# Kernel tuning notes

Measured on AMD Instinct MI355X. Metric: run time of the kernel, lower is better.

## Reference

```python
import jax, jax.numpy as jnp
import numpy as np
import math

NB = 4           # num_bands
EPS = 1e-5       # LayerNorm eps


def _dwconv(x, w):
    # depthwise Conv1d, padding=1, kernel=3. x: [b, t, c], w: [c, 1, k]
    c = x.shape[-1]
    y = jax.lax.conv_general_dilated(
        x.transpose(0, 2, 1), w, window_strides=(1,), padding=[(1, 1)],
        dimension_numbers=('NCH', 'OIH', 'NCH'), feature_group_count=c)
    return y.transpose(0, 2, 1)


def _ln(x, g, b):
    m = jnp.mean(x, axis=-1, keepdims=True)
    v = jnp.mean(jnp.square(x - m), axis=-1, keepdims=True)
    return (x - m) * jax.lax.rsqrt(v + EPS) * g + b


def _attn(x, mem, qw, qc, kw, kc, vw, vc, ow, pw, prev_qk):
    # x, mem: [b, w, c]
    b, w, c = x.shape
    d = c // NB
    q = _dwconv(x @ qw.T, qc).reshape(b, w, NB, d).transpose(0, 2, 1, 3)      # [b,nb,w,d]
    k = _dwconv(mem @ kw.T, kc).reshape(b, w, NB, d).transpose(0, 2, 3, 1)    # [b,nb,d,w]
    v = _dwconv(mem @ vw.T, vc).reshape(b, w, NB, d).transpose(0, 2, 1, 3)    # [b,nb,w,d]
    # skewed relative-position bias: matmul + pad + transpose + slice
    p = jnp.einsum('bnwd,dt->bnwt', q, pw[:, :w])                              # [b,nb,w,w]
    p = jnp.pad(p, ((0, 0), (0, 0), (0, 0), (1, 0)))                           # pad last dim left
    p = p.transpose(0, 1, 3, 2)[:, :, 1:, :]                                   # skew
    qk = (jnp.einsum('bnwd,bndt->bnwt', q, k) + p) / math.sqrt(c)
    if prev_qk is not None:
        qk = qk + prev_qk
    a = jnp.einsum('bnwt,bntd->bnwd', jax.nn.softmax(qk, axis=-1), v)
    a = a.transpose(0, 2, 1, 3).reshape(b, w, c)
    return a @ ow.T, qk


def setup_inputs() -> dict:
    key = jax.random.key(0)
    ks = jax.random.split(key, 32)
    B, CH, BINS, W, FF = 4, 8, 1024, 1024, 2048
    s = 0.02
    inp = {
        'x': jax.random.normal(ks[0], (B, CH, BINS, W), jnp.float32),
        'mem': jax.random.normal(ks[1], (B, CH, BINS, W), jnp.float32),
        'prev_qk1': jax.random.normal(ks[2], (B, NB, W, W), jnp.float32),
        'prev_qk2': jax.random.normal(ks[3], (B, NB, W, W), jnp.float32),
        'ip_w': jax.random.normal(ks[4], (CH,), jnp.float32) * s,
        'ip_b': jnp.zeros((1,), jnp.float32),
        'mp_w': jax.random.normal(ks[5], (CH,), jnp.float32) * s,
        'mp_b': jnp.zeros((1,), jnp.float32),
        'ln1_g': jnp.ones((BINS,), jnp.float32), 'ln1_b': jnp.zeros((BINS,), jnp.float32),
        'ln2_g': jnp.ones((BINS,), jnp.float32), 'ln2_b': jnp.zeros((BINS,), jnp.float32),
        'ln3_g': jnp.ones((BINS,), jnp.float32), 'ln3_b': jnp.zeros((BINS,), jnp.float32),
        'a1_qw': jax.random.normal(ks[6], (BINS, BINS), jnp.float32) * s,
        'a1_qc': jax.random.normal(ks[7], (BINS, 1, 3), jnp.float32) * 0.3,
        'a1_kw': jax.random.normal(ks[8], (BINS, BINS), jnp.float32) * s,
        'a1_kc': jax.random.normal(ks[9], (BINS, 1, 3), jnp.float32) * 0.3,
        'a1_vw': jax.random.normal(ks[10], (BINS, BINS), jnp.float32) * s,
        'a1_vc': jax.random.normal(ks[11], (BINS, 1, 3), jnp.float32) * 0.3,
        'a1_ow': jax.random.normal(ks[12], (BINS, BINS), jnp.float32) * s,
        'a1_pw': jax.random.normal(ks[13], (BINS // NB, W), jnp.float32),
        'a2_qw': jax.random.normal(ks[14], (BINS, BINS), jnp.float32) * s,
        'a2_qc': jax.random.normal(ks[15], (BINS, 1, 3), jnp.float32) * 0.3,
        'a2_kw': jax.random.normal(ks[16], (BINS, BINS), jnp.float32) * s,
        'a2_kc': jax.random.normal(ks[17], (BINS, 1, 3), jnp.float32) * 0.3,
        'a2_vw': jax.random.normal(ks[18], (BINS, BINS), jnp.float32) * s,
        'a2_vc': jax.random.normal(ks[19], (BINS, 1, 3), jnp.float32) * 0.3,
        'a2_ow': jax.random.normal(ks[20], (BINS, BINS), jnp.float32) * s,
        'a2_pw': jax.random.normal(ks[21], (BINS // NB, W), jnp.float32),
        'l1_w': jax.random.normal(ks[22], (FF, BINS), jnp.float32) * s,
        'l2_w': jax.random.normal(ks[23], (BINS, FF), jnp.float32) * s,
    }
    return inp


def reference(x, mem, prev_qk1, prev_qk2, ip_w, ip_b, mp_w, mp_b,
              ln1_g, ln1_b, ln2_g, ln2_b, ln3_g, ln3_b,
              a1_qw, a1_qc, a1_kw, a1_kc, a1_vw, a1_vc, a1_ow, a1_pw,
              a2_qw, a2_qc, a2_kw, a2_kc, a2_vw, a2_vc, a2_ow, a2_pw,
              l1_w, l2_w):
    # 1x1 Conv2d to 1 channel then [b, w, bins] layout
    xs = jnp.einsum('bchw,c->bwh', x, ip_w) + ip_b    # [b, w, bins]
    ms = jnp.einsum('bchw,c->bwh', mem, mp_w) + mp_b
    # self-attention with prev_qk residual
    h, qk1 = _attn(_ln(xs, ln1_g, ln1_b), _ln(xs, ln1_g, ln1_b),
                   a1_qw, a1_qc, a1_kw, a1_kc, a1_vw, a1_vc, a1_ow, a1_pw, prev_qk1)
    xs = xs + h
    # cross-attention against mem
    h, qk2 = _attn(_ln(xs, ln2_g, ln2_b), ms,
                   a2_qw, a2_qc, a2_kw, a2_kc, a2_vw, a2_vc, a2_ow, a2_pw, prev_qk2)
    xs = xs + h
    # squared-ReLU FFN
    h = _ln(xs, ln3_g, ln3_b)
    h = jnp.square(jax.nn.relu(h @ l1_w.T)) @ l2_w.T
    xs = xs + h
    out = xs.transpose(0, 2, 1)[:, None]              # [b, 1, bins, w]
    return (out, qk1, qk2)
```

## Files before the change

kernel.cpp:

```cpp
#include <hip/hip_runtime.h>
#include <stdint.h>

typedef unsigned short u16;
typedef __bf16 bfv8 __attribute__((ext_vector_type(8)));
typedef float f32x4 __attribute__((ext_vector_type(4)));
typedef unsigned short u16x8 __attribute__((ext_vector_type(8)));

#define DI __device__ __forceinline__

DI u16 f2bf(float f) {
  union { float f; unsigned u; } c; c.f = f;
  unsigned r = c.u + 0x7FFFu + ((c.u >> 16) & 1u);
  return (u16)(r >> 16);
}
DI float bf2f(u16 b) {
  union { unsigned u; float f; } c; c.u = ((unsigned)b) << 16;
  return c.f;
}

enum { EPI_BF16 = 0, EPI_RELU2 = 1, EPI_ADDF32 = 2, EPI_QK = 3 };

#define GLDS(g, l)                                                              \
  __builtin_amdgcn_global_load_lds((const __attribute__((address_space(1))) void*)(g), \
                                   (__attribute__((address_space(3))) void*)(l), 16, 0, 0)

#define VMCNT_BAR(N)                                        \
  do {                                                      \
    asm volatile("s_waitcnt vmcnt(" #N ")" ::: "memory");   \
    __builtin_amdgcn_sched_barrier(0);                      \
    __builtin_amdgcn_s_barrier();                           \
    __builtin_amdgcn_sched_barrier(0);                      \
  } while (0)

#define BAR_ONLY()                                          \
  do {                                                      \
    __builtin_amdgcn_sched_barrier(0);                      \
    __builtin_amdgcn_s_barrier();                           \
    __builtin_amdgcn_sched_barrier(0);                      \
  } while (0)

template <int EPI, bool KSPLIT>
__global__ __launch_bounds__(512, 4) void gemm128(
    const u16* __restrict__ Aq, const u16* __restrict__ Akv, int asplit,
    long a1q, long a1r, int lda1,
    const u16* __restrict__ A2, int lda2,
    const u16* __restrict__ B1, long b1q, long b1r, int ldb1,
    const u16* __restrict__ B2, long b2q, long b2r, int ldb2,
    int K, int ksp,
    void* __restrict__ Cv, long cq, long cr, int ldc,
    const float* __restrict__ extra, long eq, int lde,
    float scale)
{
  constexpr int NJ = 2;
  constexpr int SS = 16384;
  __shared__ __align__(16) u16 lds[2 * SS];
  const int tid = threadIdx.x;
  const int wid = tid >> 6, lane = tid & 63;

  const int gx = gridDim.x, gy = gridDim.y;
  const int nwg = gx * gy * (int)gridDim.z;
  const int flat = blockIdx.x + gx * (blockIdx.y + gy * blockIdx.z);
  const int q = nwg >> 3, r = nwg & 7;
  const int xcd = flat & 7, idx = flat >> 3;
  const int wg = (xcd < r ? xcd * (q + 1) : r * (q + 1) + (xcd - r) * q) + idx;
  const int bx = wg % gx;
  const int tmp = wg / gx;
  const int by = tmp % gy;
  const int bz = tmp / gy;

  const long zq = bz >> 2, zr = bz & 3;
  const int m0 = by * 128, n0 = bx * 128;
  const u16* Ab = ((n0 >= asplit) ? Akv : Aq) + zq * a1q + zr * a1r;
  const u16* Bb = B1 + zq * b1q + zr * b1r;
  const u16* B2b = KSPLIT ? (B2 + zq * b2q + zr * b2r) : (const u16*)nullptr;
  const int wm = (wid >> 2) * 64, wn = (wid & 3) * 32;
  const int fr = lane & 15, fq = lane >> 4;

  f32x4 acc[4][NJ];
#pragma unroll
  for (int i = 0; i < 4; ++i)
#pragma unroll
    for (int j = 0; j < NJ; ++j)
      acc[i][j] = (f32x4){0.f, 0.f, 0.f, 0.f};

  const int nt = K >> 6;

  auto STAGE = [&](int tt, int sb) {
    const int k0 = tt << 6;
    u16* Ld = &lds[sb * SS];
    const u16* Asrc; int la; const u16* Bsrc; int lb;
    if (!KSPLIT || k0 < ksp) { Asrc = Ab + k0; la = lda1; Bsrc = Bb + k0; lb = ldb1; }
    else { Asrc = A2 + (k0 - ksp); la = lda2; Bsrc = B2b + (k0 - ksp); lb = ldb2; }
#pragma unroll
    for (int l = 0; l < 2; ++l) {
      int idx2 = (l << 9) + tid;
      int row = idx2 >> 3;
      int sc = ((idx2 & 7) ^ (row & 7)) << 3;
      GLDS(Asrc + (size_t)(m0 + row) * la + sc,
           Ld + (((l << 3) + wid) << 9));
    }
#pragma unroll
    for (int l = 0; l < 2; ++l) {
      int idx2 = (l << 9) + tid;
      int row = idx2 >> 3;
      int sc = ((idx2 & 7) ^ (row & 7)) << 3;
      GLDS(Bsrc + (size_t)(n0 + row) * lb + sc,
           Ld + 8192 + (((l << 3) + wid) << 9));
    }
  };

  auto COMPUTE = [&](int cb) {
    const u16* As = &lds[cb * SS];
    const u16* Bs = As + 8192;
#pragma unroll
    for (int ks = 0; ks < 2; ++ks) {
      bfv8 av[4];
#pragma unroll
      for (int i = 0; i < 4; ++i) {
        int ra = wm + i * 16 + fr;
        int ca = (((ks << 2) + fq) ^ (ra & 7)) << 3;
        av[i] = *(const bfv8*)&As[(ra << 6) + ca];
      }
      bfv8 bv[2];
#pragma unroll
      for (int j = 0; j < 2; ++j) {
        int rb = wn + (j << 4) + fr;
        int cb2 = (((ks << 2) + fq) ^ (rb & 7)) << 3;
        bv[j] = *(const bfv8*)&Bs[(rb << 6) + cb2];
      }
      __builtin_amdgcn_s_setprio(1);
#pragma unroll
      for (int i = 0; i < 4; ++i) {
        acc[i][0] = __builtin_amdgcn_mfma_f32_16x16x32_bf16(av[i], bv[0], acc[i][0], 0, 0, 0);
        acc[i][1] = __builtin_amdgcn_mfma_f32_16x16x32_bf16(av[i], bv[1], acc[i][1], 0, 0, 0);
      }
      __builtin_amdgcn_s_setprio(0);
    }
  };

  STAGE(0, 0);
  STAGE(1, 1);
  VMCNT_BAR(4);
  for (int t = 0; t < nt; ++t) {
    COMPUTE(t & 1);
    BAR_ONLY();
    if (t + 2 < nt) {
      STAGE(t + 2, t & 1);
      VMCNT_BAR(4);
    } else if (t + 1 < nt) {
      VMCNT_BAR(0);
    }
  }

  if constexpr (EPI == EPI_BF16 || EPI == EPI_RELU2) {
    u16* Cb = (u16*)Cv + zq * cq + zr * cr;
#pragma unroll
    for (int i = 0; i < 4; ++i)
#pragma unroll
      for (int j = 0; j < NJ; ++j)
#pragma unroll
        for (int r2 = 0; r2 < 4; ++r2) {
          int row = m0 + wm + i * 16 + (fq << 2) + r2;
          int col = n0 + wn + j * 16 + fr;
          float v = acc[i][j][r2];
          if constexpr (EPI == EPI_RELU2) { v = fmaxf(v, 0.f); v = v * v; }
          Cb[(size_t)row * ldc + col] = f2bf(v);
        }
  } else if constexpr (EPI == EPI_ADDF32) {
    float* Cb = (float*)Cv + zq * cq + zr * cr;
#pragma unroll
    for (int i = 0; i < 4; ++i)
#pragma unroll
      for (int j = 0; j < NJ; ++j)
#pragma unroll
        for (int r2 = 0; r2 < 4; ++r2) {
          int row = m0 + wm + i * 16 + (fq << 2) + r2;
          int col = n0 + wn + j * 16 + fr;
          Cb[(size_t)row * ldc + col] += acc[i][j][r2];
        }
  } else {
    float* Cb = (float*)Cv + zq * cq + zr * cr;
    const float* Eb = extra + (size_t)bz * eq;
#pragma unroll
    for (int i = 0; i < 4; ++i)
#pragma unroll
      for (int j = 0; j < NJ; ++j)
#pragma unroll
        for (int r2 = 0; r2 < 4; ++r2) {
          int row = m0 + wm + i * 16 + (fq << 2) + r2;
          int col = n0 + wn + j * 16 + fr;
          Cb[(size_t)row * ldc + col] = acc[i][j][r2] * scale + Eb[(size_t)row * lde + col];
        }
  }
}

__global__ __launch_bounds__(256) void proj4_kernel(const float* __restrict__ x,
                                                    const float* __restrict__ memp,
                                                    const float* __restrict__ ipw,
                                                    const float* __restrict__ ipb,
                                                    const float* __restrict__ mpw,
                                                    const float* __restrict__ mpb,
                                                    float* __restrict__ xs,
                                                    u16* __restrict__ msb)
{
  __shared__ __align__(16) float sbuf[2][16][256];
  const int t = threadIdx.x;
  const int wid = t >> 6, lane = t & 63;
  const int task = blockIdx.z >> 2;
  const int b = blockIdx.z & 3;
  const int h0 = blockIdx.x << 4;
  const int w0 = blockIdx.y << 8;
  const float* src = task ? memp : x;
  const float* w8 = task ? mpw : ipw;
  const float bias = task ? mpb[0] : ipb[0];
  const int crot = (blockIdx.x + blockIdx.y + blockIdx.z) & 7;
  float wr[8];
#pragma unroll
  for (int j = 0; j < 8; ++j) wr[j] = w8[(j + crot) & 7];
  float acc[16];
#pragma unroll
  for (int h = 0; h < 16; ++h) acc[h] = bias;
  const size_t bbase = ((size_t)b * 8) << 20;

  auto STAGE_C = [&](int i, int sb) {
    const int c = (i + crot) & 7;
    const float* g = src + bbase + ((size_t)c << 20) + (size_t)h0 * 1024 + w0 + (lane << 2);
#pragma unroll
    for (int l = 0; l < 4; ++l) {
      int row = (wid << 2) + l;
      GLDS(g + (size_t)row * 1024, &sbuf[sb][row][0]);
    }
  };

  STAGE_C(0, 0);
  STAGE_C(1, 1);
#pragma unroll
  for (int i = 0; i < 8; ++i) {
    if (i < 7) VMCNT_BAR(4); else VMCNT_BAR(0);
    {
      const float wc = wr[i];
      const int sb = i & 1;
#pragma unroll
      for (int h = 0; h < 16; ++h)
        acc[h] += sbuf[sb][h][t] * wc;
    }
    BAR_ONLY();
    if (i + 2 < 8) STAGE_C(i + 2, i & 1);
  }

  if (task) {
    u16* d = &msb[((size_t)b * 1024 + w0 + t) * 1024 + h0];
    u16x8 o0, o1;
#pragma unroll
    for (int h = 0; h < 8; ++h) { o0[h] = f2bf(acc[h]); o1[h] = f2bf(acc[h + 8]); }
    *(u16x8*)&d[0] = o0;
    *(u16x8*)&d[8] = o1;
  } else {
    float* d = &xs[((size_t)b * 1024 + w0 + t) * 1024 + h0];
#pragma unroll
    for (int p = 0; p < 4; ++p) {
      f32x4 v = {acc[p * 4], acc[p * 4 + 1], acc[p * 4 + 2], acc[p * 4 + 3]};
      *(f32x4*)&d[p * 4] = v;
    }
  }
}

__global__ __launch_bounds__(256) void ln_kernel(const float* __restrict__ x,
                                                 const float* __restrict__ g,
                                                 const float* __restrict__ b,
                                                 u16* __restrict__ out)
{
  int row = blockIdx.x, tid = threadIdx.x;
  float4 v = ((const float4*)(x + (size_t)row * 1024))[tid];
  float s = v.x + v.y + v.z + v.w;
  float s2 = v.x * v.x + v.y * v.y + v.z * v.z + v.w * v.w;
#pragma unroll
  for (int o = 32; o; o >>= 1) { s += __shfl_down(s, o); s2 += __shfl_down(s2, o); }
  __shared__ float rs[4], rs2[4];
  int wid = tid >> 6, lane = tid & 63;
  if (lane == 0) { rs[wid] = s; rs2[wid] = s2; }
  __syncthreads();
  s = rs[0] + rs[1] + rs[2] + rs[3];
  s2 = rs2[0] + rs2[1] + rs2[2] + rs2[3];
  float mean = s * (1.f / 1024.f);
  float var = s2 * (1.f / 1024.f) - mean * mean;
  float rstd = rsqrtf(var + 1e-5f);
  float4 gv = ((const float4*)g)[tid];
  float4 bv = ((const float4*)b)[tid];
  ushort4 o;
  o.x = f2bf((v.x - mean) * rstd * gv.x + bv.x);
  o.y = f2bf((v.y - mean) * rstd * gv.y + bv.y);
  o.z = f2bf((v.z - mean) * rstd * gv.z + bv.z);
  o.w = f2bf((v.w - mean) * rstd * gv.w + bv.w);
  ((ushort4*)out)[(size_t)row * 256 + tid] = o;
}

__global__ __launch_bounds__(128) void dwconv_qk_kernel(const u16* __restrict__ qkv,
                                                        const float* __restrict__ qc,
                                                        const float* __restrict__ kc,
                                                        u16* __restrict__ Qc,
                                                        u16* __restrict__ Kc)
{
  int sel = blockIdx.y;
  int row = blockIdx.x;
  int t = row & 1023;
  int c0 = threadIdx.x * 8;
  const u16* r0 = qkv + (size_t)row * 3072 + (sel << 10) + c0;
  const float* wc = sel ? kc : qc;
  u16* dst = (sel ? Kc : Qc) + (size_t)row * 1024 + c0;
  u16x8 zv = {0, 0, 0, 0, 0, 0, 0, 0};
  u16x8 xm = zv, xp = zv;
  if (t > 0) xm = *(const u16x8*)(r0 - 3072);
  u16x8 xc = *(const u16x8*)r0;
  if (t < 1023) xp = *(const u16x8*)(r0 + 3072);
  u16x8 o;
#pragma unroll
  for (int j = 0; j < 8; ++j) {
    int c = c0 + j;
    float v = bf2f(xm[j]) * wc[c * 3 + 0] + bf2f(xc[j]) * wc[c * 3 + 1] + bf2f(xp[j]) * wc[c * 3 + 2];
    o[j] = f2bf(v);
  }
  *(u16x8*)dst = o;
}

__global__ __launch_bounds__(1024) void dwconv_t_kernel(const u16* __restrict__ qkv,
                                                        const float* __restrict__ wc,
                                                        u16* __restrict__ out)
{
  __shared__ float tile[32][33];
  int b = blockIdx.z;
  int t = blockIdx.x * 32 + threadIdx.y;
  int c = blockIdx.y * 32 + threadIdx.x;
  size_t base = ((size_t)b * 1024 + t) * 3072 + 2048 + c;
  float xm = (t > 0) ? bf2f(qkv[base - 3072]) : 0.f;
  float xc = bf2f(qkv[base]);
  float xp = (t < 1023) ? bf2f(qkv[base + 3072]) : 0.f;
  tile[threadIdx.y][threadIdx.x] = xm * wc[c * 3 + 0] + xc * wc[c * 3 + 1] + xp * wc[c * 3 + 2];
  __syncthreads();
  int c2 = blockIdx.y * 32 + threadIdx.y;
  int t2 = blockIdx.x * 32 + threadIdx.x;
  int z = b * 4 + (c2 >> 8);
  out[((size_t)z * 256 + (c2 & 255)) * 1024 + t2] = f2bf(tile[threadIdx.x][threadIdx.y]);
}

__global__ __launch_bounds__(256) void softmax_kernel(const float* __restrict__ qk,
                                                      u16* __restrict__ P)
{
  size_t row = blockIdx.x;
  int tid = threadIdx.x;
  float4 v = ((const float4*)(qk + row * 1024))[tid];
  float m = fmaxf(fmaxf(v.x, v.y), fmaxf(v.z, v.w));
#pragma unroll
  for (int o = 32; o; o >>= 1) m = fmaxf(m, __shfl_down(m, o));
  __shared__ float red[4];
  int wid = tid >> 6, lane = tid & 63;
  if (lane == 0) red[wid] = m;
  __syncthreads();
  m = fmaxf(fmaxf(red[0], red[1]), fmaxf(red[2], red[3]));
  float e0 = __expf(v.x - m), e1 = __expf(v.y - m), e2 = __expf(v.z - m), e3 = __expf(v.w - m);
  float s = e0 + e1 + e2 + e3;
#pragma unroll
  for (int o = 32; o; o >>= 1) s += __shfl_down(s, o);
  __syncthreads();
  if (lane == 0) red[wid] = s;
  __syncthreads();
  s = red[0] + red[1] + red[2] + red[3];
  float rinv = 1.f / s;
  ushort4 o;
  o.x = f2bf(e0 * rinv); o.y = f2bf(e1 * rinv); o.z = f2bf(e2 * rinv); o.w = f2bf(e3 * rinv);
  ((ushort4*)P)[row * 256 + tid] = o;
}

struct CastJobs { const float* s[12]; u16* d[12]; };
__global__ __launch_bounds__(256) void cast12_kernel(CastJobs J)
{
  int j = blockIdx.y;
  int i = blockIdx.x * 256 + threadIdx.x;
  float4 v = ((const float4*)J.s[j])[i];
  ushort4 o;
  o.x = f2bf(v.x); o.y = f2bf(v.y); o.z = f2bf(v.z); o.w = f2bf(v.w);
  ((ushort4*)J.d[j])[i] = o;
}

__global__ __launch_bounds__(1024) void pwt_kernel(const float* __restrict__ pw,
                                                   u16* __restrict__ pwT)
{
  __shared__ float tile[32][33];
  int d = blockIdx.y * 32 + threadIdx.y;
  int t = blockIdx.x * 32 + threadIdx.x;
  tile[threadIdx.y][threadIdx.x] = pw[(size_t)d * 1024 + t];
  __syncthreads();
  int t2 = blockIdx.x * 32 + threadIdx.y;
  int d2 = blockIdx.y * 32 + threadIdx.x;
  pwT[(size_t)t2 * 256 + d2] = f2bf(tile[threadIdx.x][threadIdx.y]);
}

__global__ __launch_bounds__(1024) void tout_kernel(const float* __restrict__ xs,
                                                    float* __restrict__ out)
{
  __shared__ float tile[32][33];
  int b = blockIdx.z;
  int w = blockIdx.x * 32 + threadIdx.y;
  int h = blockIdx.y * 32 + threadIdx.x;
  tile[threadIdx.y][threadIdx.x] = xs[((size_t)b * 1024 + w) * 1024 + h];
  __syncthreads();
  int h2 = blockIdx.y * 32 + threadIdx.y;
  int w2 = blockIdx.x * 32 + threadIdx.x;
  out[((size_t)b * 1024 + h2) * 1024 + w2] = tile[threadIdx.x][threadIdx.y];
}

static void run_attn(hipStream_t stream, float* xs, const u16* qsrc, const u16* kvsrc, int asplit,
                     u16* QKVraw, u16* Qc, u16* Kc, u16* Vt, u16* P, u16* Am,
                     const u16* wqkv, const u16* wo, const u16* pwt,
                     const float* qc, const float* kc, const float* vc,
                     const float* prevqk, float* qko)
{
  dim3 blk(512);
  gemm128<EPI_BF16, false><<<dim3(24, 32, 1), blk, 0, stream>>>(
      qsrc, kvsrc, asplit, 0, 0, 1024, nullptr, 0,
      wqkv, 0, 0, 1024, nullptr, 0, 0, 0,
      1024, 0, QKVraw, 0, 0, 3072, nullptr, 0, 0, 1.f);
  dwconv_qk_kernel<<<dim3(4096, 2), 128, 0, stream>>>(QKVraw, qc, kc, Qc, Kc);
  dwconv_t_kernel<<<dim3(32, 32, 4), dim3(32, 32), 0, stream>>>(QKVraw, vc, Vt);
  gemm128<EPI_QK, true><<<dim3(8, 8, 16), blk, 0, stream>>>(
      Qc, Qc, 1 << 30, 1048576, 256, 1024, pwt, 256,
      Kc, 1048576, 256, 1024, Qc, 1048576, 256, 1024,
      512, 256, qko, 4194304, 1048576, 1024, prevqk, 1048576, 1024, 0.03125f);
  softmax_kernel<<<16384, 256, 0, stream>>>(qko, P);
  gemm128<EPI_BF16, false><<<dim3(2, 8, 16), blk, 0, stream>>>(
      P, P, 1 << 30, 4194304, 1048576, 1024, nullptr, 0,
      Vt, 1048576, 262144, 1024, nullptr, 0, 0, 0,
      1024, 0, Am, 1048576, 256, 1024, nullptr, 0, 0, 1.f);
  gemm128<EPI_ADDF32, false><<<dim3(8, 32, 1), blk, 0, stream>>>(
      Am, Am, 1 << 30, 0, 0, 1024, nullptr, 0,
      wo, 0, 0, 1024, nullptr, 0, 0, 0,
      1024, 0, xs, 0, 0, 1024, nullptr, 0, 0, 1.f);
}

extern "C" void kernel_launch(void* const* d_in, const int* in_sizes, int n_in,
                              void* d_out, int out_size, void* d_ws, size_t ws_size,
                              hipStream_t stream)
{
  (void)in_sizes; (void)n_in; (void)out_size; (void)ws_size;
  const float* x    = (const float*)d_in[0];
  const float* memp = (const float*)d_in[1];
  const float* pqk1 = (const float*)d_in[2];
  const float* pqk2 = (const float*)d_in[3];
  const float* ip_w = (const float*)d_in[4];
  const float* ip_b = (const float*)d_in[5];
  const float* mp_w = (const float*)d_in[6];
  const float* mp_b = (const float*)d_in[7];
  const float* ln1g = (const float*)d_in[8];
  const float* ln1b = (const float*)d_in[9];
  const float* ln2g = (const float*)d_in[10];
  const float* ln2b = (const float*)d_in[11];
  const float* ln3g = (const float*)d_in[12];
  const float* ln3b = (const float*)d_in[13];
  const float* a1qw = (const float*)d_in[14];
  const float* a1qc = (const float*)d_in[15];
  const float* a1kw = (const float*)d_in[16];
  const float* a1kc = (const float*)d_in[17];
  const float* a1vw = (const float*)d_in[18];
  const float* a1vc = (const float*)d_in[19];
  const float* a1ow = (const float*)d_in[20];
  const float* a1pw = (const float*)d_in[21];
  const float* a2qw = (const float*)d_in[22];
  const float* a2qc = (const float*)d_in[23];
  const float* a2kw = (const float*)d_in[24];
  const float* a2kc = (const float*)d_in[25];
  const float* a2vw = (const float*)d_in[26];
  const float* a2vc = (const float*)d_in[27];
  const float* a2ow = (const float*)d_in[28];
  const float* a2pw = (const float*)d_in[29];
  const float* l1w  = (const float*)d_in[30];
  const float* l2w  = (const float*)d_in[31];

  float* outp = (float*)d_out;
  float* qk1o = outp + 4194304;
  float* qk2o = outp + 20971520;

  const size_t MB = 1024 * 1024;
  char* W = (char*)d_ws;
  float* xs   = (float*)(W);
  u16* msb    = (u16*)(W + 16 * MB);
  u16* xln    = (u16*)(W + 24 * MB);
  u16* QKVraw = (u16*)(W + 32 * MB);
  u16* Qc     = (u16*)(W + 56 * MB);
  u16* Kc     = (u16*)(W + 64 * MB);
  u16* Vt     = (u16*)(W + 72 * MB);
  u16* P      = (u16*)(W + 80 * MB);
  u16* Am     = (u16*)(W + 112 * MB);
  u16* wqkv1  = (u16*)(W + 120 * MB);
  u16* wqkv2  = (u16*)(W + 126 * MB);
  u16* wo1    = (u16*)(W + 132 * MB);
  u16* wo2    = (u16*)(W + 134 * MB);
  u16* wl1    = (u16*)(W + 136 * MB);
  u16* wl2    = (u16*)(W + 140 * MB);
  u16* pwt1   = (u16*)(W + 144 * MB);
  u16* pwt2   = (u16*)(W + 144 * MB + 512 * 1024);
  u16* H1     = QKVraw;

  CastJobs J;
  J.s[0] = a1qw; J.d[0] = wqkv1;
  J.s[1] = a1kw; J.d[1] = wqkv1 + 1048576;
  J.s[2] = a1vw; J.d[2] = wqkv1 + 2097152;
  J.s[3] = a2qw; J.d[3] = wqkv2;
  J.s[4] = a2kw; J.d[4] = wqkv2 + 1048576;
  J.s[5] = a2vw; J.d[5] = wqkv2 + 2097152;
  J.s[6] = a1ow; J.d[6] = wo1;
  J.s[7] = a2ow; J.d[7] = wo2;
  J.s[8] = l1w;            J.d[8] = wl1;
  J.s[9] = l1w + 1048576;  J.d[9] = wl1 + 1048576;
  J.s[10] = l2w;           J.d[10] = wl2;
  J.s[11] = l2w + 1048576; J.d[11] = wl2 + 1048576;
  cast12_kernel<<<dim3(1024, 12), 256, 0, stream>>>(J);
  pwt_kernel<<<dim3(32, 8, 1), dim3(32, 32), 0, stream>>>(a1pw, pwt1);
  pwt_kernel<<<dim3(32, 8, 1), dim3(32, 32), 0, stream>>>(a2pw, pwt2);

  proj4_kernel<<<dim3(64, 4, 8), 256, 0, stream>>>(
      x, memp, ip_w, ip_b, mp_w, mp_b, xs, msb);

  ln_kernel<<<4096, 256, 0, stream>>>(xs, ln1g, ln1b, xln);
  run_attn(stream, xs, xln, xln, 1 << 30, QKVraw, Qc, Kc, Vt, P, Am,
           wqkv1, wo1, pwt1, a1qc, a1kc, a1vc, pqk1, qk1o);

  ln_kernel<<<4096, 256, 0, stream>>>(xs, ln2g, ln2b, xln);
  run_attn(stream, xs, xln, msb, 1024, QKVraw, Qc, Kc, Vt, P, Am,
           wqkv2, wo2, pwt2, a2qc, a2kc, a2vc, pqk2, qk2o);

  ln_kernel<<<4096, 256, 0, stream>>>(xs, ln3g, ln3b, xln);
  gemm128<EPI_RELU2, false><<<dim3(16, 32, 1), dim3(512), 0, stream>>>(
      xln, xln, 1 << 30, 0, 0, 1024, nullptr, 0,
      wl1, 0, 0, 1024, nullptr, 0, 0, 0,
      1024, 0, H1, 0, 0, 2048, nullptr, 0, 0, 1.f);
  gemm128<EPI_ADDF32, false><<<dim3(8, 32, 1), dim3(512), 0, stream>>>(
      H1, H1, 1 << 30, 0, 0, 2048, nullptr, 0,
      wl2, 0, 0, 2048, nullptr, 0, 0, 0,
      2048, 0, xs, 0, 0, 1024, nullptr, 0, 0, 1.f);

  tout_kernel<<<dim3(32, 32, 4), dim3(32, 32), 0, stream>>>(xs, outp);
}
```

Baseline: 475.7 us.

## Fuse softmax into the PV matmul, computing probabilities on the fly

Replaces the separate softmax kernel and the P·V GEMM with one kernel. Each wave computes row max and sum from the fp32 scores, then recomputes the exponentials while feeding MFMA with V staged through double-buffered LDS. This removes the bf16 P buffer write and read and one launch. In exchange the scores are read twice from global memory, the A operand comes straight from global memory, and only 256 blocks run.

Measured after the change: 496.0 us. 4.3% more time.

```diff
diff --git a/kernel.cpp b/kernel.cpp
--- a/kernel.cpp
+++ b/kernel.cpp
@@ -192,6 +192,103 @@
           Cb[(size_t)row * ldc + col] = acc[i][j][r2] * scale + Eb[(size_t)row * lde + col];
         }
   }
+}
+
+__global__ __launch_bounds__(256) void fsm_pv_kernel(const float* __restrict__ qko,
+                                                     const u16* __restrict__ Vt,
+                                                     u16* __restrict__ Am)
+{
+  __shared__ __align__(16) u16 Vbuf[2][16384];
+  const int t = threadIdx.x;
+  const int w = t >> 6, lane = t & 63;
+  const int z = blockIdx.y, rb = blockIdx.x;
+  const int fr = lane & 15, fq = lane >> 4;
+  const float* Q = qko + (size_t)z * 1048576;
+  const u16* Vz = Vt + (size_t)z * 262144;
+  const int r0w = rb * 64 + w * 16;
+
+  auto STAGEV = [&](int kt, int sb) {
+    const int k0 = kt << 6;
+#pragma unroll
+    for (int i8 = 0; i8 < 8; ++i8) {
+      int cidx = (((i8 << 2) + w) << 6) + lane;
+      int d = cidx >> 3, kc = cidx & 7;
+      GLDS(Vz + (size_t)d * 1024 + k0 + ((kc ^ (d & 7)) << 3),
+           &Vbuf[sb][((i8 << 2) + w) << 9]);
+    }
+  };
+
+  STAGEV(0, 0);
+  STAGEV(1, 1);
+
+  float m_mine = 0.f, r_mine = 0.f;
+#pragma unroll
+  for (int rr = 0; rr < 16; ++rr) {
+    const float* row = Q + (size_t)(r0w + rr) * 1024;
+    f32x4 v[4];
+#pragma unroll
+    for (int i = 0; i < 4; ++i) v[i] = *(const f32x4*)&row[i * 256 + lane * 4];
+    float m = v[0].x;
+#pragma unroll
+    for (int i = 0; i < 4; ++i)
+      m = fmaxf(m, fmaxf(fmaxf(v[i].x, v[i].y), fmaxf(v[i].z, v[i].w)));
+#pragma unroll
+    for (int off = 32; off; off >>= 1) m = fmaxf(m, __shfl_xor(m, off));
+    float s = 0.f;
+#pragma unroll
+    for (int i = 0; i < 4; ++i)
+      s += __expf(v[i].x - m) + __expf(v[i].y - m) + __expf(v[i].z - m) + __expf(v[i].w - m);
+#pragma unroll
+    for (int off = 32; off; off >>= 1) s += __shfl_xor(s, off);
+    if (rr == fr) { m_mine = m; r_mine = 1.f / s; }
+  }
+
+  f32x4 acc[16];
+#pragma unroll
+  for (int nf = 0; nf < 16; ++nf) acc[nf] = (f32x4){0.f, 0.f, 0.f, 0.f};
+
+  const float* arow = Q + (size_t)(r0w + fr) * 1024 + fq * 8;
+
+  for (int kt = 0; kt < 16; ++kt) {
+    if (kt < 15) VMCNT_BAR(8); else VMCNT_BAR(0);
+    const u16* Vb = &Vbuf[kt & 1][0];
+#pragma unroll
+    for (int ks = 0; ks < 2; ++ks) {
+      f32x4 a0 = *(const f32x4*)&arow[kt * 64 + ks * 32 + 0];
+      f32x4 a1 = *(const f32x4*)&arow[kt * 64 + ks * 32 + 4];
+      union { u16x8 u; bfv8 b; } cvt;
+      cvt.u[0] = f2bf(__expf(a0.x - m_mine) * r_mine);
+      cvt.u[1] = f2bf(__expf(a0.y - m_mine) * r_mine);
+      cvt.u[2] = f2bf(__expf(a0.z - m_mine) * r_mine);
+      cvt.u[3] = f2bf(__expf(a0.w - m_mine) * r_mine);
+      cvt.u[4] = f2bf(__expf(a1.x - m_mine) * r_mine);
+      cvt.u[5] = f2bf(__expf(a1.y - m_mine) * r_mine);
+      cvt.u[6] = f2bf(__expf(a1.z - m_mine) * r_mine);
+      cvt.u[7] = f2bf(__expf(a1.w - m_mine) * r_mine);
+      bfv8 av = cvt.b;
+      __builtin_amdgcn_s_setprio(1);
+#pragma unroll
+      for (int nf = 0; nf < 16; ++nf) {
+        int d = (nf << 4) + fr;
+        int g = (ks << 2) + fq;
+        bfv8 bv = *(const bfv8*)&Vb[(d << 6) + ((g ^ (d & 7)) << 3)];
+        acc[nf] = __builtin_amdgcn_mfma_f32_16x16x32_bf16(av, bv, acc[nf], 0, 0, 0);
+      }
+      __builtin_amdgcn_s_setprio(0);
+    }
+    BAR_ONLY();
+    if (kt + 2 < 16) STAGEV(kt + 2, kt & 1);
+  }
+
+  const int b = z >> 2, n = z & 3;
+  u16* Ao = Am + (size_t)b * 1048576 + n * 256;
+#pragma unroll
+  for (int nf = 0; nf < 16; ++nf)
+#pragma unroll
+    for (int r2 = 0; r2 < 4; ++r2) {
+      int row = r0w + (fq << 2) + r2;
+      Ao[(size_t)row * 1024 + (nf << 4) + fr] = f2bf(acc[nf][r2]);
+    }
 }
 
 __global__ __launch_bounds__(256) void proj4_kernel(const float* __restrict__ x,
@@ -343,34 +440,6 @@
   out[((size_t)z * 256 + (c2 & 255)) * 1024 + t2] = f2bf(tile[threadIdx.x][threadIdx.y]);
 }
 
-__global__ __launch_bounds__(256) void softmax_kernel(const float* __restrict__ qk,
-                                                      u16* __restrict__ P)
-{
-  size_t row = blockIdx.x;
-  int tid = threadIdx.x;
-  float4 v = ((const float4*)(qk + row * 1024))[tid];
-  float m = fmaxf(fmaxf(v.x, v.y), fmaxf(v.z, v.w));
-#pragma unroll
-  for (int o = 32; o; o >>= 1) m = fmaxf(m, __shfl_down(m, o));
-  __shared__ float red[4];
-  int wid = tid >> 6, lane = tid & 63;
-  if (lane == 0) red[wid] = m;
-  __syncthreads();
-  m = fmaxf(fmaxf(red[0], red[1]), fmaxf(red[2], red[3]));
-  float e0 = __expf(v.x - m), e1 = __expf(v.y - m), e2 = __expf(v.z - m), e3 = __expf(v.w - m);
-  float s = e0 + e1 + e2 + e3;
-#pragma unroll
-  for (int o = 32; o; o >>= 1) s += __shfl_down(s, o);
-  __syncthreads();
-  if (lane == 0) red[wid] = s;
-  __syncthreads();
-  s = red[0] + red[1] + red[2] + red[3];
-  float rinv = 1.f / s;
-  ushort4 o;
-  o.x = f2bf(e0 * rinv); o.y = f2bf(e1 * rinv); o.z = f2bf(e2 * rinv); o.w = f2bf(e3 * rinv);
-  ((ushort4*)P)[row * 256 + tid] = o;
-}
-
 struct CastJobs { const float* s[12]; u16* d[12]; };
 __global__ __launch_bounds__(256) void cast12_kernel(CastJobs J)
 {
@@ -410,7 +479,7 @@
 }
 
 static void run_attn(hipStream_t stream, float* xs, const u16* qsrc, const u16* kvsrc, int asplit,
-                     u16* QKVraw, u16* Qc, u16* Kc, u16* Vt, u16* P, u16* Am,
+                     u16* QKVraw, u16* Qc, u16* Kc, u16* Vt, u16* Am,
                      const u16* wqkv, const u16* wo, const u16* pwt,
                      const float* qc, const float* kc, const float* vc,
                      const float* prevqk, float* qko)
@@ -426,11 +495,7 @@
       Qc, Qc, 1 << 30, 1048576, 256, 1024, pwt, 256,
       Kc, 1048576, 256, 1024, Qc, 1048576, 256, 1024,
       512, 256, qko, 4194304, 1048576, 1024, prevqk, 1048576, 1024, 0.03125f);
-  softmax_kernel<<<16384, 256, 0, stream>>>(qko, P);
-  gemm128<EPI_BF16, false><<<dim3(2, 8, 16), blk, 0, stream>>>(
-      P, P, 1 << 30, 4194304, 1048576, 1024, nullptr, 0,
-      Vt, 1048576, 262144, 1024, nullptr, 0, 0, 0,
-      1024, 0, Am, 1048576, 256, 1024, nullptr, 0, 0, 1.f);
+  fsm_pv_kernel<<<dim3(16, 16), 256, 0, stream>>>(qko, Vt, Am);
   gemm128<EPI_ADDF32, false><<<dim3(8, 32, 1), blk, 0, stream>>>(
       Am, Am, 1 << 30, 0, 0, 1024, nullptr, 0,
       wo, 0, 0, 1024, nullptr, 0, 0, 0,
@@ -488,7 +553,6 @@
   u16* Qc     = (u16*)(W + 56 * MB);
   u16* Kc     = (u16*)(W + 64 * MB);
   u16* Vt     = (u16*)(W + 72 * MB);
-  u16* P      = (u16*)(W + 80 * MB);
   u16* Am     = (u16*)(W + 112 * MB);
   u16* wqkv1  = (u16*)(W + 120 * MB);
   u16* wqkv2  = (u16*)(W + 126 * MB);
@@ -521,11 +585,11 @@
       x, memp, ip_w, ip_b, mp_w, mp_b, xs, msb);
 
   ln_kernel<<<4096, 256, 0, stream>>>(xs, ln1g, ln1b, xln);
-  run_attn(stream, xs, xln, xln, 1 << 30, QKVraw, Qc, Kc, Vt, P, Am,
+  run_attn(stream, xs, xln, xln, 1 << 30, QKVraw, Qc, Kc, Vt, Am,
            wqkv1, wo1, pwt1, a1qc, a1kc, a1vc, pqk1, qk1o);
 
   ln_kernel<<<4096, 256, 0, stream>>>(xs, ln2g, ln2b, xln);
-  run_attn(stream, xs, xln, msb, 1024, QKVraw, Qc, Kc, Vt, P, Am,
+  run_attn(stream, xs, xln, msb, 1024, QKVraw, Qc, Kc, Vt, Am,
            wqkv2, wo2, pwt2, a2qc, a2kc, a2vc, pqk2, qk2o);
 
   ln_kernel<<<4096, 256, 0, stream>>>(xs, ln3g, ln3b, xln);
```
